# Kernel tuning notes

Measured on AMD Instinct MI355X. Metric: run time of the kernel, lower is better.

Reference implementation:

```python
import jax, jax.numpy as jnp
import numpy as np

NEG_BIG = -9e15
LRELU_SLOPE = 0.2  # torch LeakyReLU default used for act_att


def setup_inputs() -> dict:
    key = jax.random.key(0)
    k1, k2, k3, k4 = jax.random.split(key, 4)
    B, N, F_in, F_out = 8, 2048, 128, 64
    inp = jax.random.normal(k1, (B, N, F_in), dtype=jnp.float32)
    adj = jax.random.randint(k2, (N, N), 0, 2, dtype=jnp.int32)
    W = jax.random.normal(k3, (F_in, F_out), dtype=jnp.float32) * (1.0 / np.sqrt(F_in))
    a = jax.random.normal(k4, (2 * F_out, 1), dtype=jnp.float32) * (1.0 / np.sqrt(2 * F_out))
    return {"input": inp, "adj": adj, "W": W, "a": a}


def reference(input, adj, W, a):
    # h: [B, N, F_out]
    h = jnp.einsum('bnf,fo->bno', input, W)
    F_out = W.shape[1]
    a1 = a[:F_out, 0]   # [F_out] -- applied to source node i
    a2 = a[F_out:, 0]   # [F_out] -- applied to target node j
    # e[b,i,j] = leaky_relu(h_i . a1 + h_j . a2); equivalent to cat([h_i,h_j]) @ a
    s1 = h @ a1          # [B, N]
    s2 = h @ a2          # [B, N]
    e = jax.nn.leaky_relu(s1[:, :, None] + s2[:, None, :], negative_slope=LRELU_SLOPE)
    masked = jnp.where(adj[None, :, :] > 0, e, NEG_BIG)
    attention = jax.nn.softmax(masked, axis=-1)  # [B, N, N]
    # dropout p=0.0 (eval) -> identity
    h_prime = jnp.einsum('bij,bjo->bio', attention, h)
    out = jax.nn.relu(h_prime)  # concat=True -> apply act_gat
    return out, attention[..., None]
```

## Files before the change

kernel.cpp:

```cpp
#include <hip/hip_runtime.h>
#include <hip/hip_bf16.h>

constexpr int B = 8, N = 2048, FIN = 128, FOUT = 64;

typedef __attribute__((ext_vector_type(8))) short short8;
typedef __attribute__((ext_vector_type(4))) float f32x4;

__device__ __forceinline__ unsigned int pk_bf16(float lo, float hi) {
    union { __hip_bfloat162 h2; unsigned int u; } c;
    c.h2 = __float22bfloat162_rn(float2{lo, hi});
    return c.u;
}
__device__ __forceinline__ unsigned short f2bf(float f) {
    return (unsigned short)(pk_bf16(f, 0.f) & 0xFFFFu);
}

__global__ __launch_bounds__(512, 2) void kA(
        const float* __restrict__ inp, const float* __restrict__ W,
        const float* __restrict__ a, const int* __restrict__ adj,
        unsigned short* __restrict__ hP, float* __restrict__ s1,
        float* __restrict__ s2, unsigned long long* __restrict__ adjbits) {
    __shared__ float wa1l[128], wa2l[128];
    __shared__ unsigned short wT[64][136];
    __shared__ unsigned short aT[128][136];

    int bx = blockIdx.x, t = threadIdx.x, w = t >> 6, lane = t & 63;

    if (bx >= 128) {
        int row = (bx - 128) * 8 + w;
        const int* ar = adj + (size_t)row * N;
        unsigned long long* br = adjbits + (size_t)row * 32;
        #pragma unroll 8
        for (int wq = 0; wq < 32; ++wq) {
            unsigned long long m = __ballot(ar[wq * 64 + lane] > 0);
            if (lane == 0) br[wq] = m;
        }
        return;
    }

    int b = bx >> 4, i0 = (bx & 15) * 128;

    if (t < 128) {
        const float* wr = W + t * FOUT;
        float acc1 = 0.f;
        #pragma unroll 16
        for (int o = 0; o < 64; ++o) acc1 = fmaf(wr[o], a[o], acc1);
        wa1l[t] = acc1;
    } else if (t < 256) {
        int k = t - 128;
        const float* wr = W + k * FOUT;
        float acc2 = 0.f;
        #pragma unroll 16
        for (int o = 0; o < 64; ++o) acc2 = fmaf(wr[o], a[64 + o], acc2);
        wa2l[k] = acc2;
    } else {
        int t2 = t - 256;
        int o = t2 & 63, kg = t2 >> 6;
        #pragma unroll 8
        for (int kk = 0; kk < 32; ++kk) {
            int k = kg * 32 + kk;
            wT[o][k] = f2bf(W[k * FOUT + o]);
        }
    }
    __syncthreads();

    {
        int row = t >> 2, seg = t & 3;
        const float* ip = inp + ((size_t)b * N + i0 + row) * FIN + seg * 32;
        float s1p = 0.f, s2p = 0.f;
        #pragma unroll
        for (int q = 0; q < 8; ++q) {
            float4 v = *(const float4*)&ip[q * 4];
            int k = seg * 32 + q * 4;
            s1p += v.x * wa1l[k] + v.y * wa1l[k + 1] + v.z * wa1l[k + 2] + v.w * wa1l[k + 3];
            s2p += v.x * wa2l[k] + v.y * wa2l[k + 1] + v.z * wa2l[k + 2] + v.w * wa2l[k + 3];
            unsigned int* dst = (unsigned int*)&aT[row][k];
            dst[0] = pk_bf16(v.x, v.y);
            dst[1] = pk_bf16(v.z, v.w);
        }
        s1p += __shfl_xor(s1p, 1); s1p += __shfl_xor(s1p, 2);
        s2p += __shfl_xor(s2p, 1); s2p += __shfl_xor(s2p, 2);
        if (seg == 0) {
            s1[(size_t)b * N + i0 + row] = s1p;
            s2[(size_t)b * N + i0 + row] = s2p;
        }
    }
    __syncthreads();

    int r = lane & 15, g = lane >> 4;
    int mloc = w * 16;
    f32x4 acc[4];
    #pragma unroll
    for (int nf = 0; nf < 4; ++nf)
        #pragma unroll
        for (int q = 0; q < 4; ++q) acc[nf][q] = 0.f;
    #pragma unroll
    for (int ks = 0; ks < 4; ++ks) {
        short8 Af = *(const short8*)&aT[mloc + r][ks * 32 + g * 8];
        #pragma unroll
        for (int nf = 0; nf < 4; ++nf) {
            short8 Bf = *(const short8*)&wT[nf * 16 + r][ks * 32 + g * 8];
            acc[nf] = __builtin_amdgcn_mfma_f32_16x16x32_bf16(Af, Bf, acc[nf], 0, 0, 0);
        }
    }
    __syncthreads();

    #pragma unroll
    for (int nf = 0; nf < 4; ++nf)
        #pragma unroll
        for (int q = 0; q < 4; ++q)
            aT[mloc + g * 4 + q][nf * 16 + r] = f2bf(acc[nf][q]);
    __syncthreads();

    #pragma unroll
    for (int half = 0; half < 2; ++half) {
        int idx = t + half * 512;
        int kb_l = idx >> 8, nf = (idx >> 6) & 3, ln = idx & 63;
        int g2 = ln >> 4, r2 = ln & 15;
        union { short8 s8; unsigned short u[8]; } tw;
        #pragma unroll
        for (int e = 0; e < 8; ++e)
            tw.u[e] = aT[kb_l * 32 + g2 * 8 + e][nf * 16 + r2];
        int kbg = (bx & 15) * 4 + kb_l;
        *(short8*)&hP[((((size_t)b * 64 + kbg) * 4 + nf) << 9) + ln * 8] = tw.s8;
    }
}

__global__ __launch_bounds__(256, 2) void k2a_pv(
        const float* __restrict__ s1g, const float* __restrict__ s2g,
        const unsigned long long* __restrict__ adjbits,
        const unsigned short* __restrict__ hP,
        float* __restrict__ rvg, float* __restrict__ out) {
    __shared__ float s2l[N];
    __shared__ float s1l[16];
    __shared__ float ps[4][16];
    __shared__ float rvl[16];
    __shared__ float red[3][16][68];

    int L = blockIdx.x;
    int b = L & 7, m0 = (L >> 3) * 16;
    int t = threadIdx.x, kc = t >> 6, lane = t & 63;
    int r = lane & 15, g = lane >> 4;

    {
        int j = t * 8;
        *(float4*)&s2l[j]     = *(const float4*)&s2g[(size_t)b * N + j];
        *(float4*)&s2l[j + 4] = *(const float4*)&s2g[(size_t)b * N + j + 4];
    }
    if (t < 16) s1l[t] = s1g[(size_t)b * N + m0 + t];
    __syncthreads();

    float s1v = s1l[r];
    const unsigned long long* brow = adjbits + (size_t)(m0 + r) * 32 + kc * 8;
    const unsigned short* hpb = hP + (size_t)b * 64 * 4 * 512;

    f32x4 acc[4];
    #pragma unroll
    for (int nf = 0; nf < 4; ++nf)
        #pragma unroll
        for (int q = 0; q < 4; ++q) acc[nf][q] = 0.f;
    float rsum = 0.f;

    #pragma unroll 1
    for (int so = 0; so < 4; ++so) {
        unsigned long long bw0 = brow[so * 2];
        unsigned long long bw1 = brow[so * 2 + 1];
        #pragma unroll
        for (int si = 0; si < 4; ++si) {
            int st = so * 4 + si;
            int jb = kc * 512 + st * 32 + g * 8;
            unsigned long long bwv = (si < 2) ? bw0 : bw1;
            unsigned int bits = (unsigned int)(bwv >> ((si & 1) * 32 + g * 8)) & 0xFFu;
            float4 sA = *(const float4*)&s2l[jb];
            float4 sB = *(const float4*)&s2l[jb + 4];
            union { short8 s8; unsigned int d[4]; } pk;
            {
                float xa, xb, pa, pb;
                xa = s1v + sA.x; xa = fmaxf(xa, 0.2f * xa);
                xb = s1v + sA.y; xb = fmaxf(xb, 0.2f * xb);
                pa = (bits & 1u) ? __expf(xa) : 0.f;
                pb = (bits & 2u) ? __expf(xb) : 0.f;
                rsum += pa + pb; pk.d[0] = pk_bf16(pa, pb);
                xa = s1v + sA.z; xa = fmaxf(xa, 0.2f * xa);
                xb = s1v + sA.w; xb = fmaxf(xb, 0.2f * xb);
                pa = (bits & 4u) ? __expf(xa) : 0.f;
                pb = (bits & 8u) ? __expf(xb) : 0.f;
                rsum += pa + pb; pk.d[1] = pk_bf16(pa, pb);
                xa = s1v + sB.x; xa = fmaxf(xa, 0.2f * xa);
                xb = s1v + sB.y; xb = fmaxf(xb, 0.2f * xb);
                pa = (bits & 16u) ? __expf(xa) : 0.f;
                pb = (bits & 32u) ? __expf(xb) : 0.f;
                rsum += pa + pb; pk.d[2] = pk_bf16(pa, pb);
                xa = s1v + sB.z; xa = fmaxf(xa, 0.2f * xa);
                xb = s1v + sB.w; xb = fmaxf(xb, 0.2f * xb);
                pa = (bits & 64u) ? __expf(xa) : 0.f;
                pb = (bits & 128u) ? __expf(xb) : 0.f;
                rsum += pa + pb; pk.d[3] = pk_bf16(pa, pb);
            }
            int kb = kc * 16 + st;
            const unsigned short* hs = hpb + (((size_t)kb * 4) << 9) + lane * 8;
            #pragma unroll
            for (int nf = 0; nf < 4; ++nf) {
                short8 Bf = *(const short8*)&hs[nf << 9];
                acc[nf] = __builtin_amdgcn_mfma_f32_16x16x32_bf16(pk.s8, Bf, acc[nf], 0, 0, 0);
            }
        }
    }
    rsum += __shfl_xor(rsum, 16);
    rsum += __shfl_xor(rsum, 32);
    if (lane < 16) ps[kc][r] = rsum;
    if (kc > 0) {
        #pragma unroll
        for (int nf = 0; nf < 4; ++nf)
            #pragma unroll
            for (int q = 0; q < 4; ++q)
                red[kc - 1][4 * g + q][nf * 16 + r] = acc[nf][q];
    }
    __syncthreads();
    if (t < 16) {
        float rv = 1.0f / (ps[0][t] + ps[1][t] + ps[2][t] + ps[3][t]);
        rvl[t] = rv;
        rvg[(size_t)b * N + m0 + t] = rv;
    }
    __syncthreads();
    if (kc == 0) {
        #pragma unroll
        for (int nf = 0; nf < 4; ++nf) {
            #pragma unroll
            for (int q = 0; q < 4; ++q) {
                int m = 4 * g + q;
                int o = nf * 16 + r;
                float vv = acc[nf][q] + red[0][m][o] + red[1][m][o] + red[2][m][o];
                vv *= rvl[m];
                out[((size_t)b * N + m0 + m) * FOUT + o] = vv > 0.f ? vv : 0.f;
            }
        }
    }
}

__global__ __launch_bounds__(256, 8) void k2b_att(
        const float* __restrict__ s1g, const float* __restrict__ s2g,
        const unsigned long long* __restrict__ adjbits,
        const float* __restrict__ rvg, float* __restrict__ att) {
    int i = blockIdx.x;
    int t = threadIdx.x, w = t >> 6, lane = t & 63;
    int b = blockIdx.y * 4 + w;
    const unsigned long long* brow = adjbits + (size_t)i * 32;
    float s1v = s1g[(size_t)b * N + i];
    float rv  = rvg[(size_t)b * N + i];
    const float* s2b = s2g + (size_t)b * N;
    float* orow = att + ((size_t)b * N + i) * N;
    #pragma unroll
    for (int it = 0; it < 8; ++it) {
        int j = it * 256 + lane * 4;
        unsigned int bits = (unsigned int)(brow[j >> 6] >> (j & 63)) & 0xFu;
        float4 sv = *(const float4*)&s2b[j];
        float x0 = s1v + sv.x; x0 = fmaxf(x0, 0.2f * x0);
        float x1 = s1v + sv.y; x1 = fmaxf(x1, 0.2f * x1);
        float x2 = s1v + sv.z; x2 = fmaxf(x2, 0.2f * x2);
        float x3 = s1v + sv.w; x3 = fmaxf(x3, 0.2f * x3);
        float4 o;
        o.x = (bits & 1u) ? __expf(x0) * rv : 0.f;
        o.y = (bits & 2u) ? __expf(x1) * rv : 0.f;
        o.z = (bits & 4u) ? __expf(x2) * rv : 0.f;
        o.w = (bits & 8u) ? __expf(x3) * rv : 0.f;
        *(float4*)&orow[j] = o;
    }
}

extern "C" void kernel_launch(void* const* d_in, const int* in_sizes, int n_in,
                              void* d_out, int out_size, void* d_ws, size_t ws_size,
                              hipStream_t stream) {
    const float* inp = (const float*)d_in[0];
    const int*   adj = (const int*)d_in[1];
    const float* W   = (const float*)d_in[2];
    const float* a   = (const float*)d_in[3];

    float* out = (float*)d_out;
    float* att = out + (size_t)B * N * FOUT;

    unsigned short* hP = (unsigned short*)d_ws;
    float* s1  = (float*)(hP + (size_t)B * FOUT * N);
    float* s2  = s1 + (size_t)B * N;
    float* rvg = s2 + (size_t)B * N;
    unsigned long long* adjbits = (unsigned long long*)(rvg + (size_t)B * N);

    kA<<<384, 512, 0, stream>>>(inp, W, a, adj, hP, s1, s2, adjbits);
    k2a_pv<<<1024, 256, 0, stream>>>(s1, s2, adjbits, hP, rvg, out);
    dim3 g2b(N, 2);
    k2b_att<<<g2b, 256, 0, stream>>>(s1, s2, adjbits, rvg, att);
}
```

Before: 60.00 us.

## Fuse attention-matrix writer into PV kernel with interleaved heterogeneous blocks

After: 73.97 us. 23.3% more time.

```diff
diff --git a/kernel.cpp b/kernel.cpp
--- a/kernel.cpp
+++ b/kernel.cpp
@@ -126,20 +126,68 @@
     }
 }
 
-__global__ __launch_bounds__(256, 2) void k2a_pv(
+__global__ __launch_bounds__(256, 2) void k2(
         const float* __restrict__ s1g, const float* __restrict__ s2g,
         const unsigned long long* __restrict__ adjbits,
         const unsigned short* __restrict__ hP,
-        float* __restrict__ rvg, float* __restrict__ out) {
+        float* __restrict__ att, float* __restrict__ out) {
     __shared__ float s2l[N];
     __shared__ float s1l[16];
     __shared__ float ps[4][16];
     __shared__ float rvl[16];
     __shared__ float red[3][16][68];
 
-    int L = blockIdx.x;
+    int bx = blockIdx.x;
+    int t = threadIdx.x, w = t >> 6, lane = t & 63;
+
+    if (bx % 5 != 4) {
+        int ai = (bx / 5) * 4 + (bx % 5);
+        int i = ai >> 1;
+        int b = (ai & 1) * 4 + w;
+        const unsigned long long* brow = adjbits + (size_t)i * 32;
+        float s1v = s1g[(size_t)b * N + i];
+        const float* s2b = s2g + (size_t)b * N;
+        float* orow = att + ((size_t)b * N + i) * N;
+        float rsum = 0.f;
+        #pragma unroll
+        for (int it = 0; it < 8; ++it) {
+            int j = it * 256 + lane * 4;
+            unsigned int bits = (unsigned int)(brow[j >> 6] >> (j & 63)) & 0xFu;
+            float4 sv = *(const float4*)&s2b[j];
+            float x0 = s1v + sv.x; x0 = fmaxf(x0, 0.2f * x0);
+            float x1 = s1v + sv.y; x1 = fmaxf(x1, 0.2f * x1);
+            float x2 = s1v + sv.z; x2 = fmaxf(x2, 0.2f * x2);
+            float x3 = s1v + sv.w; x3 = fmaxf(x3, 0.2f * x3);
+            rsum += (bits & 1u) ? __expf(x0) : 0.f;
+            rsum += (bits & 2u) ? __expf(x1) : 0.f;
+            rsum += (bits & 4u) ? __expf(x2) : 0.f;
+            rsum += (bits & 8u) ? __expf(x3) : 0.f;
+        }
+        #pragma unroll
+        for (int off = 1; off < 64; off <<= 1) rsum += __shfl_xor(rsum, off);
+        float rv = 1.0f / rsum;
+        #pragma unroll
+        for (int it = 0; it < 8; ++it) {
+            int j = it * 256 + lane * 4;
+            unsigned int bits = (unsigned int)(brow[j >> 6] >> (j & 63)) & 0xFu;
+            float4 sv = *(const float4*)&s2b[j];
+            float x0 = s1v + sv.x; x0 = fmaxf(x0, 0.2f * x0);
+            float x1 = s1v + sv.y; x1 = fmaxf(x1, 0.2f * x1);
+            float x2 = s1v + sv.z; x2 = fmaxf(x2, 0.2f * x2);
+            float x3 = s1v + sv.w; x3 = fmaxf(x3, 0.2f * x3);
+            float4 o;
+            o.x = (bits & 1u) ? __expf(x0) * rv : 0.f;
+            o.y = (bits & 2u) ? __expf(x1) * rv : 0.f;
+            o.z = (bits & 4u) ? __expf(x2) * rv : 0.f;
+            o.w = (bits & 8u) ? __expf(x3) * rv : 0.f;
+            *(float4*)&orow[j] = o;
+        }
+        return;
+    }
+
+    int L = bx / 5;
     int b = L & 7, m0 = (L >> 3) * 16;
-    int t = threadIdx.x, kc = t >> 6, lane = t & 63;
+    int kc = w;
     int r = lane & 15, g = lane >> 4;
 
     {
@@ -217,11 +265,8 @@
                 red[kc - 1][4 * g + q][nf * 16 + r] = acc[nf][q];
     }
     __syncthreads();
-    if (t < 16) {
-        float rv = 1.0f / (ps[0][t] + ps[1][t] + ps[2][t] + ps[3][t]);
-        rvl[t] = rv;
-        rvg[(size_t)b * N + m0 + t] = rv;
-    }
+    if (t < 16)
+        rvl[t] = 1.0f / (ps[0][t] + ps[1][t] + ps[2][t] + ps[3][t]);
     __syncthreads();
     if (kc == 0) {
         #pragma unroll
@@ -238,36 +283,6 @@
     }
 }
 
-__global__ __launch_bounds__(256, 8) void k2b_att(
-        const float* __restrict__ s1g, const float* __restrict__ s2g,
-        const unsigned long long* __restrict__ adjbits,
-        const float* __restrict__ rvg, float* __restrict__ att) {
-    int i = blockIdx.x;
-    int t = threadIdx.x, w = t >> 6, lane = t & 63;
-    int b = blockIdx.y * 4 + w;
-    const unsigned long long* brow = adjbits + (size_t)i * 32;
-    float s1v = s1g[(size_t)b * N + i];
-    float rv  = rvg[(size_t)b * N + i];
-    const float* s2b = s2g + (size_t)b * N;
-    float* orow = att + ((size_t)b * N + i) * N;
-    #pragma unroll
-    for (int it = 0; it < 8; ++it) {
-        int j = it * 256 + lane * 4;
-        unsigned int bits = (unsigned int)(brow[j >> 6] >> (j & 63)) & 0xFu;
-        float4 sv = *(const float4*)&s2b[j];
-        float x0 = s1v + sv.x; x0 = fmaxf(x0, 0.2f * x0);
-        float x1 = s1v + sv.y; x1 = fmaxf(x1, 0.2f * x1);
-        float x2 = s1v + sv.z; x2 = fmaxf(x2, 0.2f * x2);
-        float x3 = s1v + sv.w; x3 = fmaxf(x3, 0.2f * x3);
-        float4 o;
-        o.x = (bits & 1u) ? __expf(x0) * rv : 0.f;
-        o.y = (bits & 2u) ? __expf(x1) * rv : 0.f;
-        o.z = (bits & 4u) ? __expf(x2) * rv : 0.f;
-        o.w = (bits & 8u) ? __expf(x3) * rv : 0.f;
-        *(float4*)&orow[j] = o;
-    }
-}
-
 extern "C" void kernel_launch(void* const* d_in, const int* in_sizes, int n_in,
                               void* d_out, int out_size, void* d_ws, size_t ws_size,
                               hipStream_t stream) {
@@ -282,11 +297,8 @@
     unsigned short* hP = (unsigned short*)d_ws;
     float* s1  = (float*)(hP + (size_t)B * FOUT * N);
     float* s2  = s1 + (size_t)B * N;
-    float* rvg = s2 + (size_t)B * N;
-    unsigned long long* adjbits = (unsigned long long*)(rvg + (size_t)B * N);
+    unsigned long long* adjbits = (unsigned long long*)(s2 + (size_t)B * N);
 
     kA<<<384, 512, 0, stream>>>(inp, W, a, adj, hP, s1, s2, adjbits);
-    k2a_pv<<<1024, 256, 0, stream>>>(s1, s2, adjbits, hP, rvg, out);
-    dim3 g2b(N, 2);
-    k2b_att<<<g2b, 256, 0, stream>>>(s1, s2, adjbits, rvg, att);
-}
+    k2<<<5120, 256, 0, stream>>>(s1, s2, adjbits, hP, att, out);
+}
```

## Fuse attention-matrix write into the PV kernel and drop separate attention kernel

Applied to the files above, without the earlier changes.

Result: faster. 53.26 us, median of 2 (-11.2%).

```diff
diff --git a/kernel.cpp b/kernel.cpp
--- a/kernel.cpp
+++ b/kernel.cpp
@@ -126,11 +126,11 @@
     }
 }
 
-__global__ __launch_bounds__(256, 2) void k2a_pv(
+__global__ __launch_bounds__(256, 2) void k2_fused(
         const float* __restrict__ s1g, const float* __restrict__ s2g,
         const unsigned long long* __restrict__ adjbits,
         const unsigned short* __restrict__ hP,
-        float* __restrict__ rvg, float* __restrict__ out) {
+        float* __restrict__ att, float* __restrict__ out) {
     __shared__ float s2l[N];
     __shared__ float s1l[16];
     __shared__ float ps[4][16];
@@ -217,12 +217,10 @@
                 red[kc - 1][4 * g + q][nf * 16 + r] = acc[nf][q];
     }
     __syncthreads();
-    if (t < 16) {
-        float rv = 1.0f / (ps[0][t] + ps[1][t] + ps[2][t] + ps[3][t]);
-        rvl[t] = rv;
-        rvg[(size_t)b * N + m0 + t] = rv;
-    }
-    __syncthreads();
+    if (t < 16)
+        rvl[t] = 1.0f / (ps[0][t] + ps[1][t] + ps[2][t] + ps[3][t]);
+    __syncthreads();
+
     if (kc == 0) {
         #pragma unroll
         for (int nf = 0; nf < 4; ++nf) {
@@ -236,35 +234,30 @@
             }
         }
     }
-}
-
-__global__ __launch_bounds__(256, 8) void k2b_att(
-        const float* __restrict__ s1g, const float* __restrict__ s2g,
-        const unsigned long long* __restrict__ adjbits,
-        const float* __restrict__ rvg, float* __restrict__ att) {
-    int i = blockIdx.x;
-    int t = threadIdx.x, w = t >> 6, lane = t & 63;
-    int b = blockIdx.y * 4 + w;
-    const unsigned long long* brow = adjbits + (size_t)i * 32;
-    float s1v = s1g[(size_t)b * N + i];
-    float rv  = rvg[(size_t)b * N + i];
-    const float* s2b = s2g + (size_t)b * N;
-    float* orow = att + ((size_t)b * N + i) * N;
-    #pragma unroll
-    for (int it = 0; it < 8; ++it) {
-        int j = it * 256 + lane * 4;
-        unsigned int bits = (unsigned int)(brow[j >> 6] >> (j & 63)) & 0xFu;
-        float4 sv = *(const float4*)&s2b[j];
-        float x0 = s1v + sv.x; x0 = fmaxf(x0, 0.2f * x0);
-        float x1 = s1v + sv.y; x1 = fmaxf(x1, 0.2f * x1);
-        float x2 = s1v + sv.z; x2 = fmaxf(x2, 0.2f * x2);
-        float x3 = s1v + sv.w; x3 = fmaxf(x3, 0.2f * x3);
-        float4 o;
-        o.x = (bits & 1u) ? __expf(x0) * rv : 0.f;
-        o.y = (bits & 2u) ? __expf(x1) * rv : 0.f;
-        o.z = (bits & 4u) ? __expf(x2) * rv : 0.f;
-        o.w = (bits & 8u) ? __expf(x3) * rv : 0.f;
-        *(float4*)&orow[j] = o;
+
+    #pragma unroll
+    for (int rr = 0; rr < 4; ++rr) {
+        int row = kc * 4 + rr;
+        float s1r = s1l[row];
+        float rvr = rvl[row];
+        const unsigned long long* br2 = adjbits + (size_t)(m0 + row) * 32;
+        float* orow = att + ((size_t)b * N + m0 + row) * N;
+        #pragma unroll
+        for (int it = 0; it < 8; ++it) {
+            int j = it * 256 + lane * 4;
+            unsigned int bits = (unsigned int)(br2[j >> 6] >> (j & 63)) & 0xFu;
+            float4 sv = *(const float4*)&s2l[j];
+            float x0 = s1r + sv.x; x0 = fmaxf(x0, 0.2f * x0);
+            float x1 = s1r + sv.y; x1 = fmaxf(x1, 0.2f * x1);
+            float x2 = s1r + sv.z; x2 = fmaxf(x2, 0.2f * x2);
+            float x3 = s1r + sv.w; x3 = fmaxf(x3, 0.2f * x3);
+            float4 o;
+            o.x = (bits & 1u) ? __expf(x0) * rvr : 0.f;
+            o.y = (bits & 2u) ? __expf(x1) * rvr : 0.f;
+            o.z = (bits & 4u) ? __expf(x2) * rvr : 0.f;
+            o.w = (bits & 8u) ? __expf(x3) * rvr : 0.f;
+            *(float4*)&orow[j] = o;
+        }
     }
 }
 
@@ -282,11 +275,8 @@
     unsigned short* hP = (unsigned short*)d_ws;
     float* s1  = (float*)(hP + (size_t)B * FOUT * N);
     float* s2  = s1 + (size_t)B * N;
-    float* rvg = s2 + (size_t)B * N;
-    unsigned long long* adjbits = (unsigned long long*)(rvg + (size_t)B * N);
+    unsigned long long* adjbits = (unsigned long long*)(s2 + (size_t)B * N);
 
     kA<<<384, 512, 0, stream>>>(inp, W, a, adj, hP, s1, s2, adjbits);
-    k2a_pv<<<1024, 256, 0, stream>>>(s1, s2, adjbits, hP, rvg, out);
-    dim3 g2b(N, 2);
-    k2b_att<<<g2b, 256, 0, stream>>>(s1, s2, adjbits, rvg, att);
-}
+    k2_fused<<<1024, 256, 0, stream>>>(s1, s2, adjbits, hP, att, out);
+}
```
